# Optimization experiments

Measured on AMD Instinct MI355X. Metric: run time of the kernel, lower is better.

The kernel has to match this reference:

```python
import jax, jax.numpy as jnp
import numpy as np

N_NODES = 100000
N_EDGES = 1600000
N_GRAPHS = 512
IN_CH = 128
HID = 128
OUT_CH = 1
FP_DIM = 2048


def prelu(x, a):
    return jnp.where(x > 0, x, a * x)


def setup_inputs() -> dict:
    key = jax.random.key(0)
    ks = jax.random.split(key, 16)

    def glorot(k, shape):
        lim = np.sqrt(6.0 / (shape[0] + shape[1]))
        return jax.random.uniform(k, shape, jnp.float32, -lim, lim)

    x = jax.random.normal(ks[0], (N_NODES, IN_CH), jnp.float32)
    fp = jax.random.normal(ks[1], (N_GRAPHS, FP_DIM), jnp.float32)
    edge_index = jax.random.randint(ks[2], (2, N_EDGES), 0, N_NODES, jnp.int64)
    batch = jnp.sort(jax.random.randint(ks[3], (N_NODES,), 0, N_GRAPHS, jnp.int64))

    params = {
        "W_pre": glorot(ks[4], (IN_CH, HID)),
        "b_pre": jnp.zeros((HID,), jnp.float32),
        "a_pre": jnp.full((HID,), 0.25, jnp.float32),
        "Wl1": glorot(ks[5], (HID, HID)),
        "bl1": jnp.zeros((HID,), jnp.float32),
        "Wr1": glorot(ks[6], (HID, HID)),
        "a1": jnp.full((HID,), 0.25, jnp.float32),
        "Wl2": glorot(ks[7], (HID, HID)),
        "bl2": jnp.zeros((HID,), jnp.float32),
        "Wr2": glorot(ks[8], (HID, HID)),
        "a2": jnp.full((HID,), 0.25, jnp.float32),
        "W_fp": glorot(ks[9], (FP_DIM, HID)),
        "b_fp": jnp.zeros((HID,), jnp.float32),
        "a_fp": jnp.full((HID,), 0.25, jnp.float32),
        "W_post": glorot(ks[10], (2 * HID, OUT_CH)),
        "b_post": jnp.zeros((OUT_CH,), jnp.float32),
    }
    return dict(x=x, fp=fp, edge_index=edge_index, batch=batch, **params)


def sage_conv(x, src, dst, Wl, bl, Wr):
    # aggr='sum': sum messages x[src] into dst, then lin_l(agg)+bias + lin_r(x)
    agg = jax.ops.segment_sum(x[src], dst, num_segments=N_NODES)  # [N, H]
    return agg @ Wl + bl + x @ Wr


def reference(x, fp, edge_index, batch,
              W_pre, b_pre, a_pre,
              Wl1, bl1, Wr1, a1,
              Wl2, bl2, Wr2, a2,
              W_fp, b_fp, a_fp,
              W_post, b_post):
    src, dst = edge_index[0], edge_index[1]
    # pre_mp (dropout is identity at eval)
    h = prelu(x @ W_pre + b_pre, a_pre)
    # message passing
    h = prelu(sage_conv(h, src, dst, Wl1, bl1, Wr1), a1)
    h = prelu(sage_conv(h, src, dst, Wl2, bl2, Wr2), a2)
    # global mean pool over graphs
    sums = jax.ops.segment_sum(h, batch, num_segments=N_GRAPHS)  # [G, H]
    counts = jax.ops.segment_sum(jnp.ones((h.shape[0],), h.dtype), batch,
                                 num_segments=N_GRAPHS)
    pooled = sums / jnp.maximum(counts, 1.0)[:, None]
    # fingerprint head
    fp_emb = prelu(fp @ W_fp + b_fp, a_fp)
    # post mp
    out = jnp.concatenate([pooled, fp_emb], axis=1) @ W_post + b_post
    return out
```

## Files before the change

### kernel.cpp

```cpp
#include <hip/hip_runtime.h>

#define NN 100000
#define NE 1600000
#define NG 512
#define HID 128
#define FPD 2048
#define BSHIFT 8
#define NBUK ((NN + 255) >> 8)
#define BCAP 5120
#define EPB 4096
#define EPT 16

typedef _Float16 f16;
typedef __attribute__((ext_vector_type(8))) _Float16 f16x8;
typedef __attribute__((ext_vector_type(4))) float f32x4;


__global__ __launch_bounds__(256) void bucket_scatter(const int* __restrict__ src,
                                                      const int* __restrict__ dst,
                                                      int* __restrict__ bcnt,
                                                      uint2* __restrict__ bbuf, int E) {
  __shared__ int hist[NBUK];
  __shared__ int gbase[NBUK];
  __shared__ int lbase[NBUK + 1];
  __shared__ int sc[2][512];
  __shared__ uint2 stage[EPB];
  int t = threadIdx.x;
  int e0 = blockIdx.x * EPB;
  for (int i = t; i < NBUK; i += 256) hist[i] = 0;
  __syncthreads();

  int myb[EPT], myoff[EPT];
  uint2 myp[EPT];
#pragma unroll
  for (int u = 0; u < EPT; ++u) {
    int e = e0 + u * 256 + t;
    myb[u] = -1;
    if (e < E) {
      int d = dst[e];
      int b = d >> BSHIFT;
      myp[u] = make_uint2((uint)d, (uint)src[e]);
      myb[u] = b;
      myoff[u] = atomicAdd(&hist[b], 1);
    }
  }
  __syncthreads();

  sc[0][t] = (t < NBUK) ? hist[t] : 0;
  sc[0][t + 256] = (t + 256 < NBUK) ? hist[t + 256] : 0;
  int pp = 0;
  for (int off = 1; off < 512; off <<= 1) {
    __syncthreads();
    int a0 = sc[pp][t] + ((t >= off) ? sc[pp][t - off] : 0);
    int a1 = sc[pp][t + 256] + ((t + 256 >= off) ? sc[pp][t + 256 - off] : 0);
    sc[1 - pp][t] = a0;
    sc[1 - pp][t + 256] = a1;
    pp = 1 - pp;
  }
  __syncthreads();
  if (t < NBUK) lbase[t] = (t == 0) ? 0 : sc[pp][t - 1];
  if (t + 256 < NBUK) lbase[t + 256] = sc[pp][t + 255];
  if (t == 0) lbase[NBUK] = sc[pp][NBUK - 1];
  for (int i = t; i < NBUK; i += 256)
    if (hist[i] > 0) gbase[i] = atomicAdd(&bcnt[i], hist[i]);
  __syncthreads();

#pragma unroll
  for (int u = 0; u < EPT; ++u)
    if (myb[u] >= 0) stage[lbase[myb[u]] + myoff[u]] = myp[u];
  __syncthreads();

  int total = lbase[NBUK];
  for (int j = t; j < total; j += 256) {
    int lo = 0, hi = NBUK - 1;
    while (lo < hi) {
      int mid = (lo + hi + 1) >> 1;
      if (lbase[mid] <= j) lo = mid; else hi = mid - 1;
    }
    bbuf[(size_t)lo * BCAP + gbase[lo] + (j - lbase[lo])] = stage[j];
  }
}

__global__ __launch_bounds__(256) void bucket_hist(const int* __restrict__ bcnt,
                                                   const uint2* __restrict__ bbuf,
                                                   int* __restrict__ cnt) {
  __shared__ int h[256];
  int b = blockIdx.x, t = threadIdx.x;
  h[t] = 0;
  __syncthreads();
  int n = bcnt[b];
  const uint2* bb = bbuf + (size_t)b * BCAP;
  for (int e = t; e < n; e += 256) atomicAdd(&h[bb[e].x & 255], 1);
  __syncthreads();
  int node = (b << BSHIFT) + t;
  if (node < NN) cnt[node] = h[t];
}

__global__ __launch_bounds__(256) void scan1_kernel(const int* __restrict__ cnt,
                                                    int* __restrict__ partial,
                                                    int* __restrict__ bsums, int n) {
  __shared__ int lds[256];
  int t = threadIdx.x;
  int base = blockIdx.x * 1024 + t * 4;
  int4 v = make_int4(0, 0, 0, 0);
  if (base + 3 < n) {
    v = *reinterpret_cast<const int4*>(&cnt[base]);
  } else {
    if (base     < n) v.x = cnt[base];
    if (base + 1 < n) v.y = cnt[base + 1];
    if (base + 2 < n) v.z = cnt[base + 2];
    if (base + 3 < n) v.w = cnt[base + 3];
  }
  int s = v.x + v.y + v.z + v.w;
  lds[t] = s;
  __syncthreads();
  for (int off = 1; off < 256; off <<= 1) {
    int add = (t >= off) ? lds[t - off] : 0;
    __syncthreads();
    lds[t] += add;
    __syncthreads();
  }
  int run = lds[t] - s;
  run += v.x; if (base     < n) partial[base]     = run;
  run += v.y; if (base + 1 < n) partial[base + 1] = run;
  run += v.z; if (base + 2 < n) partial[base + 2] = run;
  run += v.w; if (base + 3 < n) partial[base + 3] = run;
  if (t == 255) bsums[blockIdx.x] = lds[255];
}

__global__ __launch_bounds__(256) void scan2_kernel(int* __restrict__ bsums, int nb) {
  __shared__ int lds[256];
  int t = threadIdx.x;
  int s = (t < nb) ? bsums[t] : 0;
  lds[t] = s;
  __syncthreads();
  for (int off = 1; off < 256; off <<= 1) {
    int add = (t >= off) ? lds[t - off] : 0;
    __syncthreads();
    lds[t] += add;
    __syncthreads();
  }
  if (t < nb) bsums[t] = lds[t] - s;
}

__global__ __launch_bounds__(256) void scan3_kernel(const int* __restrict__ partial,
                                                    const int* __restrict__ bsums,
                                                    int* __restrict__ rowptr, int n) {
  int i = blockIdx.x * 256 + threadIdx.x;
  if (i == 0) rowptr[0] = 0;
  if (i < n) rowptr[i + 1] = partial[i] + bsums[i >> 10];
}

__global__ __launch_bounds__(256) void bucket_place(const int* __restrict__ bcnt,
                                                    const uint2* __restrict__ bbuf,
                                                    const int* __restrict__ rowptr,
                                                    int* __restrict__ cols) {
  __shared__ int cur[256];
  int b = blockIdx.x, t = threadIdx.x;
  int node = (b << BSHIFT) + t;
  cur[t] = rowptr[node < NN ? node : NN];
  __syncthreads();
  int n = bcnt[b];
  const uint2* bb = bbuf + (size_t)b * BCAP;
  for (int e = t; e < n; e += 256) {
    uint2 p = bb[e];
    int pos = atomicAdd(&cur[p.x & 255], 1);
    cols[pos] = (int)p.y;
  }
}


__global__ __launch_bounds__(256) void cvt_f32_f16(const float* __restrict__ x,
                                                   f16* __restrict__ xh, int n4) {
  int i = blockIdx.x * 256 + threadIdx.x;
  if (i < n4) {
    float4 v = *reinterpret_cast<const float4*>(&x[i * 4]);
    union { uint2 u; f16 h[4]; } o;
    o.h[0] = (f16)v.x; o.h[1] = (f16)v.y; o.h[2] = (f16)v.z; o.h[3] = (f16)v.w;
    *reinterpret_cast<uint2*>(&xh[i * 4]) = o.u;
  }
}

__global__ __launch_bounds__(256) void cvt_w5(const float* __restrict__ w0,
                                              const float* __restrict__ w1,
                                              const float* __restrict__ w2,
                                              const float* __restrict__ w3,
                                              const float* __restrict__ w4,
                                              f16* __restrict__ out) {
  int idx = blockIdx.x * 256 + threadIdx.x;
  if (idx >= 5 * 16384) return;
  int w = idx >> 14, rem = idx & 16383;
  int j = rem >> 7, k = rem & 127;
  const float* W = (w == 0) ? w0 : (w == 1) ? w1 : (w == 2) ? w2 : (w == 3) ? w3 : w4;
  out[idx] = (f16)W[k * 128 + j];
}

__global__ __launch_bounds__(256) void cvt_wfp(const float* __restrict__ W,
                                               f16* __restrict__ out) {
  int idx = blockIdx.x * 256 + threadIdx.x;
  if (idx >= 128 * 2048) return;
  int j = idx >> 11, k = idx & 2047;
  out[idx] = (f16)W[k * 128 + j];
}


__global__ __launch_bounds__(256) void agg_f16(const f16* __restrict__ H,
                                               const int* __restrict__ rowptr,
                                               const int* __restrict__ cols,
                                               f16* __restrict__ out) {
  int node = blockIdx.x * 4 + (threadIdx.x >> 6);
  int lane = threadIdx.x & 63;
  int s = rowptr[node], e = rowptr[node + 1];
  float a0 = 0.f, a1 = 0.f;
  union { uint u; f16 h[2]; } cv;
  int i = s;
  for (; i + 3 < e; i += 4) {
    int c0 = cols[i], c1 = cols[i + 1], c2 = cols[i + 2], c3 = cols[i + 3];
    uint u0 = *reinterpret_cast<const uint*>(&H[(size_t)c0 * 128 + lane * 2]);
    uint u1 = *reinterpret_cast<const uint*>(&H[(size_t)c1 * 128 + lane * 2]);
    uint u2 = *reinterpret_cast<const uint*>(&H[(size_t)c2 * 128 + lane * 2]);
    uint u3 = *reinterpret_cast<const uint*>(&H[(size_t)c3 * 128 + lane * 2]);
    cv.u = u0; a0 += (float)cv.h[0]; a1 += (float)cv.h[1];
    cv.u = u1; a0 += (float)cv.h[0]; a1 += (float)cv.h[1];
    cv.u = u2; a0 += (float)cv.h[0]; a1 += (float)cv.h[1];
    cv.u = u3; a0 += (float)cv.h[0]; a1 += (float)cv.h[1];
  }
  for (; i < e; ++i) {
    cv.u = *reinterpret_cast<const uint*>(&H[(size_t)cols[i] * 128 + lane * 2]);
    a0 += (float)cv.h[0]; a1 += (float)cv.h[1];
  }
  union { uint u; f16 h[2]; } pk;
  pk.h[0] = (f16)a0; pk.h[1] = (f16)a1;
  *reinterpret_cast<uint*>(&out[(size_t)node * 128 + lane * 2]) = pk.u;
}


template <int MODE>
__global__ __launch_bounds__(256) void gemm_f16(const f16* __restrict__ A1,
                                                const f16* __restrict__ A2,
                                                const f16* __restrict__ W1t,
                                                const f16* __restrict__ W2t,
                                                const float* __restrict__ bias,
                                                const float* __restrict__ pa,
                                                f16* __restrict__ Ch, int rows) {
  int t = threadIdx.x;
  int wave = t >> 6, lane = t & 63;
  int lrow = lane & 15, lk = lane >> 4;
  int r0 = blockIdx.x * 128;
  int n0 = wave << 1;

  const f16x8* Wv1 = reinterpret_cast<const f16x8*>(W1t);
  const f16x8* Wv2 = reinterpret_cast<const f16x8*>(W2t);

  f16x8 w1[2][4], w2[2][4];
#pragma unroll
  for (int ni = 0; ni < 2; ++ni)
#pragma unroll
    for (int ks = 0; ks < 4; ++ks) {
      int wi = ((((n0 + ni) << 4) + lrow) << 4) + (ks << 2) + lk;
      w1[ni][ks] = Wv1[wi];
      if (MODE >= 1) w2[ni][ks] = Wv2[wi];
    }

  float bv[2], av[2];
#pragma unroll
  for (int ni = 0; ni < 2; ++ni) {
    int col = ((n0 + ni) << 4) + lrow;
    bv[ni] = bias ? bias[col] : 0.f;
    av[ni] = pa ? pa[col] : 1.f;
  }

  f16x8 aA[2][4], aB[2][4];
  {
    int r = r0 + lrow;
    if (r > rows - 1) r = rows - 1;
    size_t off = (size_t)r * 128 + (lk << 3);
#pragma unroll
    for (int ks = 0; ks < 4; ++ks) {
      aA[0][ks] = *reinterpret_cast<const f16x8*>(A1 + off + (ks << 5));
      if (MODE >= 1) aB[0][ks] = *reinterpret_cast<const f16x8*>(A2 + off + (ks << 5));
    }
  }

#pragma unroll
  for (int rg = 0; rg < 8; ++rg) {
    int cur = rg & 1, nxt = cur ^ 1;
    if (rg < 7) {
      int rn = r0 + ((rg + 1) << 4) + lrow;
      if (rn > rows - 1) rn = rows - 1;
      size_t offn = (size_t)rn * 128 + (lk << 3);
#pragma unroll
      for (int ks = 0; ks < 4; ++ks) {
        aA[nxt][ks] = *reinterpret_cast<const f16x8*>(A1 + offn + (ks << 5));
        if (MODE >= 1) aB[nxt][ks] = *reinterpret_cast<const f16x8*>(A2 + offn + (ks << 5));
      }
    }
    f32x4 acc1[2] = {(f32x4){0.f, 0.f, 0.f, 0.f}, (f32x4){0.f, 0.f, 0.f, 0.f}};
    f32x4 acc2[2] = {(f32x4){0.f, 0.f, 0.f, 0.f}, (f32x4){0.f, 0.f, 0.f, 0.f}};
#pragma unroll
    for (int ks = 0; ks < 4; ++ks) {
#pragma unroll
      for (int ni = 0; ni < 2; ++ni) {
        acc1[ni] = __builtin_amdgcn_mfma_f32_16x16x32_f16(aA[cur][ks], w1[ni][ks], acc1[ni], 0, 0, 0);
        if (MODE >= 1)
          acc2[ni] = __builtin_amdgcn_mfma_f32_16x16x32_f16(aB[cur][ks], w2[ni][ks], acc2[ni], 0, 0, 0);
      }
    }
#pragma unroll
    for (int ni = 0; ni < 2; ++ni) {
      int col = ((n0 + ni) << 4) + lrow;
#pragma unroll
      for (int j = 0; j < 4; ++j) {
        int rr = r0 + (rg << 4) + (lk << 2) + j;
        if (rr < rows) {
          float xv = acc1[ni][j] + bv[ni];
          if (MODE >= 1) xv += acc2[ni][j];
          if (pa) xv = xv > 0.f ? xv : av[ni] * xv;
          Ch[(size_t)rr * 128 + col] = (f16)xv;
        }
      }
    }
  }
}


__global__ __launch_bounds__(256) void fp_gemm(const f16* __restrict__ A,
                                               const f16* __restrict__ Wt,
                                               float* __restrict__ part) {
  int kc = blockIdx.x;
  int rb = blockIdx.y;
  int t = threadIdx.x;
  int wave = t >> 6, lane = t & 63;
  int lrow = lane & 15, lk = lane >> 4;
  int r0 = rb * 128;
  int n0 = wave << 1;

  const f16x8* Wv = reinterpret_cast<const f16x8*>(Wt);
  const f16x8* Av = reinterpret_cast<const f16x8*>(A);

  f16x8 w[2][4];
#pragma unroll
  for (int ni = 0; ni < 2; ++ni)
#pragma unroll
    for (int ks = 0; ks < 4; ++ks) {
      int j = ((n0 + ni) << 4) + lrow;
      w[ni][ks] = Wv[j * 256 + (kc << 4) + (ks << 2) + lk];
    }

#pragma unroll 2
  for (int rg = 0; rg < 8; ++rg) {
    int r = r0 + (rg << 4) + lrow;
    f16x8 a[4];
#pragma unroll
    for (int ks = 0; ks < 4; ++ks)
      a[ks] = Av[r * 256 + (kc << 4) + (ks << 2) + lk];
    f32x4 acc[2] = {(f32x4){0.f, 0.f, 0.f, 0.f}, (f32x4){0.f, 0.f, 0.f, 0.f}};
#pragma unroll
    for (int ks = 0; ks < 4; ++ks)
#pragma unroll
      for (int ni = 0; ni < 2; ++ni)
        acc[ni] = __builtin_amdgcn_mfma_f32_16x16x32_f16(a[ks], w[ni][ks], acc[ni], 0, 0, 0);
#pragma unroll
    for (int ni = 0; ni < 2; ++ni) {
      int col = ((n0 + ni) << 4) + lrow;
#pragma unroll
      for (int j = 0; j < 4; ++j) {
        int rr = r0 + (rg << 4) + (lk << 2) + j;
        part[((size_t)kc * 512 + rr) * 128 + col] = acc[ni][j];
      }
    }
  }
}

__global__ __launch_bounds__(256) void fp_fin(const float* __restrict__ part,
                                              const float* __restrict__ bfp,
                                              const float* __restrict__ afp,
                                              float* __restrict__ femb) {
  int idx = blockIdx.x * 256 + threadIdx.x;
  if (idx >= 512 * 128) return;
  int j = idx & 127;
  float s = bfp[j];
#pragma unroll
  for (int kc = 0; kc < 16; ++kc) s += part[(size_t)kc * 65536 + idx];
  float a = afp[j];
  femb[idx] = s > 0.f ? s : a * s;
}


__device__ __forceinline__ int lower_bound_dev(const int* __restrict__ arr, int n, int val) {
  int lo = 0, hi = n;
  while (lo < hi) {
    int mid = (lo + hi) >> 1;
    if (arr[mid] < val) lo = mid + 1; else hi = mid;
  }
  return lo;
}

__global__ __launch_bounds__(512) void pool_mean(const f16* __restrict__ H,
                                                 const int* __restrict__ batch,
                                                 float* __restrict__ pooled) {
  __shared__ float red[512];
  int g = blockIdx.x;
  int t = threadIdx.x;
  int col = t & 127, rq = t >> 7;
  int start = lower_bound_dev(batch, NN, g);
  int end = lower_bound_dev(batch, NN, g + 1);
  float acc = 0.f;
  for (int r = start + rq; r < end; r += 4) acc += (float)H[(size_t)r * 128 + col];
  red[t] = acc;
  __syncthreads();
  if (rq == 0) {
    float s = red[col] + red[128 + col] + red[256 + col] + red[384 + col];
    int c = end - start;
    pooled[g * 128 + col] = s / (float)(c > 0 ? c : 1);
  }
}


__global__ __launch_bounds__(64) void final_out(const float* __restrict__ pooled,
                                                const float* __restrict__ femb,
                                                const float* __restrict__ Wp,
                                                const float* __restrict__ bp,
                                                float* __restrict__ out) {
  int g = blockIdx.x;
  int t = threadIdx.x;
  float acc = 0.f;
  for (int i = t; i < 128; i += 64)
    acc += pooled[g * 128 + i] * Wp[i] + femb[g * 128 + i] * Wp[128 + i];
  for (int off = 32; off > 0; off >>= 1) acc += __shfl_down(acc, off);
  if (t == 0) out[g] = acc + bp[0];
}


extern "C" void kernel_launch(void* const* d_in, const int* in_sizes, int n_in,
                              void* d_out, int out_size, void* d_ws, size_t ws_size,
                              hipStream_t stream) {
  const float* x      = (const float*)d_in[0];
  const float* fp     = (const float*)d_in[1];
  const int*   ei     = (const int*)d_in[2];
  const int*   batch  = (const int*)d_in[3];
  const float* W_pre  = (const float*)d_in[4];
  const float* b_pre  = (const float*)d_in[5];
  const float* a_pre  = (const float*)d_in[6];
  const float* Wl1    = (const float*)d_in[7];
  const float* bl1    = (const float*)d_in[8];
  const float* Wr1    = (const float*)d_in[9];
  const float* a1     = (const float*)d_in[10];
  const float* Wl2    = (const float*)d_in[11];
  const float* bl2    = (const float*)d_in[12];
  const float* Wr2    = (const float*)d_in[13];
  const float* a2     = (const float*)d_in[14];
  const float* W_fp   = (const float*)d_in[15];
  const float* b_fp   = (const float*)d_in[16];
  const float* a_fp   = (const float*)d_in[17];
  const float* W_post = (const float*)d_in[18];
  const float* b_post = (const float*)d_in[19];

  const int* src = ei;
  const int* dst = ei + NE;

  const size_t NBUF = (size_t)NN * 128;
  f16* buf0 = (f16*)d_ws;
  f16* buf1 = buf0 + NBUF;
  f16* buf2 = buf1 + NBUF;
  f16* buf3 = buf2 + NBUF;
  f16* Wt   = buf3 + NBUF;
  f16* fpb  = Wt + 5 * 16384;
  f16* Wfpt = fpb + 512 * 2048;
  float* part = (float*)(Wfpt + 128 * 2048);
  int* cnt     = (int*)(part + 16 * 512 * 128);
  int* rowptr  = cnt + NN;
  int* bsums   = rowptr + NN + 4;
  int* partial = bsums + 128;
  int* colsA   = partial + NN;
  int* bcnt    = colsA + NE;
  uint2* bbuf  = (uint2*)(bcnt + ((NBUK + 3) & ~3));
  float* pooled = (float*)(bbuf + (size_t)NBUK * BCAP);
  float* femb   = pooled + NG * 128;

  hipMemsetAsync(bcnt, 0, NBUK * sizeof(int), stream);
  bucket_scatter<<<(NE + EPB - 1) / EPB, 256, 0, stream>>>(src, dst, bcnt, bbuf, NE);
  bucket_hist<<<NBUK, 256, 0, stream>>>(bcnt, bbuf, cnt);
  int nb = (NN + 1023) / 1024;
  scan1_kernel<<<nb, 256, 0, stream>>>(cnt, partial, bsums, NN);
  scan2_kernel<<<1, 256, 0, stream>>>(bsums, nb);
  scan3_kernel<<<(NN + 255) / 256, 256, 0, stream>>>(partial, bsums, rowptr, NN);
  bucket_place<<<NBUK, 256, 0, stream>>>(bcnt, bbuf, rowptr, colsA);

  cvt_f32_f16<<<(NN * 128 / 4 + 255) / 256, 256, 0, stream>>>(x, buf0, NN * 128 / 4);
  cvt_w5<<<(5 * 16384 + 255) / 256, 256, 0, stream>>>(W_pre, Wl1, Wr1, Wl2, Wr2, Wt);
  cvt_f32_f16<<<(512 * 2048 / 4 + 255) / 256, 256, 0, stream>>>(fp, fpb, 512 * 2048 / 4);
  cvt_wfp<<<(128 * 2048 + 255) / 256, 256, 0, stream>>>(W_fp, Wfpt);

  const f16* Wt_pre = Wt;
  const f16* Wt_l1  = Wt + 16384;
  const f16* Wt_r1  = Wt + 32768;
  const f16* Wt_l2  = Wt + 49152;
  const f16* Wt_r2  = Wt + 65536;

  int gGemm = (NN + 127) / 128;

  gemm_f16<0><<<gGemm, 256, 0, stream>>>(buf0, nullptr, Wt_pre, nullptr,
                                         b_pre, a_pre, buf2, NN);

  {
    dim3 g(16, 4);
    fp_gemm<<<g, 256, 0, stream>>>(fpb, Wfpt, part);
    fp_fin<<<(512 * 128 + 255) / 256, 256, 0, stream>>>(part, b_fp, a_fp, femb);
  }

  agg_f16<<<NN / 4, 256, 0, stream>>>(buf2, rowptr, colsA, buf1);
  gemm_f16<1><<<gGemm, 256, 0, stream>>>(buf1, buf2, Wt_l1, Wt_r1,
                                         bl1, a1, buf3, NN);

  agg_f16<<<NN / 4, 256, 0, stream>>>(buf3, rowptr, colsA, buf0);
  gemm_f16<1><<<gGemm, 256, 0, stream>>>(buf0, buf3, Wt_l2, Wt_r2,
                                         bl2, a2, buf2, NN);

  pool_mean<<<NG, 512, 0, stream>>>(buf2, batch, pooled);
  final_out<<<NG, 64, 0, stream>>>(pooled, femb, W_post, b_post, (float*)d_out);
}
```

Baseline: 362.9 us.

## Fuse SAGE aggregation with its GEMM and fold input conversion into pre-GEMM

Each SAGEConv layer now runs as one kernel. Every block gathers neighbor sums for 64 nodes into swizzled LDS, then runs the Wl/Wr MFMA products with bias and PReLU, so the aggregated feature matrix never goes through global memory. The pre-MLP GEMM reads fp32 x directly and converts to fp16 in registers, which removes a separate conversion pass. Bucket entries are packed into 32 bits (8-bit local dst, 24-bit src), halving bucket buffer traffic but limiting node ids to fewer than 2^24. Smaller conv blocks and the loss of prefetch in the pre-GEMM may reduce overlap.

```diff
diff --git a/kernel.cpp b/kernel.cpp
--- a/kernel.cpp
+++ b/kernel.cpp
@@ -19,19 +19,19 @@
 __global__ __launch_bounds__(256) void bucket_scatter(const int* __restrict__ src,
                                                       const int* __restrict__ dst,
                                                       int* __restrict__ bcnt,
-                                                      uint2* __restrict__ bbuf, int E) {
+                                                      uint* __restrict__ bbuf, int E) {
   __shared__ int hist[NBUK];
   __shared__ int gbase[NBUK];
   __shared__ int lbase[NBUK + 1];
   __shared__ int sc[2][512];
-  __shared__ uint2 stage[EPB];
+  __shared__ uint stage[EPB];
   int t = threadIdx.x;
   int e0 = blockIdx.x * EPB;
   for (int i = t; i < NBUK; i += 256) hist[i] = 0;
   __syncthreads();
 
   int myb[EPT], myoff[EPT];
-  uint2 myp[EPT];
+  uint myp[EPT];
 #pragma unroll
   for (int u = 0; u < EPT; ++u) {
     int e = e0 + u * 256 + t;
@@ -39,7 +39,7 @@
     if (e < E) {
       int d = dst[e];
       int b = d >> BSHIFT;
-      myp[u] = make_uint2((uint)d, (uint)src[e]);
+      myp[u] = ((uint)(d & 255) << 24) | (uint)src[e];
       myb[u] = b;
       myoff[u] = atomicAdd(&hist[b], 1);
     }
@@ -82,15 +82,15 @@
 }
 
 __global__ __launch_bounds__(256) void bucket_hist(const int* __restrict__ bcnt,
-                                                   const uint2* __restrict__ bbuf,
+                                                   const uint* __restrict__ bbuf,
                                                    int* __restrict__ cnt) {
   __shared__ int h[256];
   int b = blockIdx.x, t = threadIdx.x;
   h[t] = 0;
   __syncthreads();
   int n = bcnt[b];
-  const uint2* bb = bbuf + (size_t)b * BCAP;
-  for (int e = t; e < n; e += 256) atomicAdd(&h[bb[e].x & 255], 1);
+  const uint* bb = bbuf + (size_t)b * BCAP;
+  for (int e = t; e < n; e += 256) atomicAdd(&h[bb[e] >> 24], 1);
   __syncthreads();
   int node = (b << BSHIFT) + t;
   if (node < NN) cnt[node] = h[t];
@@ -152,7 +152,7 @@
 }
 
 __global__ __launch_bounds__(256) void bucket_place(const int* __restrict__ bcnt,
-                                                    const uint2* __restrict__ bbuf,
+                                                    const uint* __restrict__ bbuf,
                                                     const int* __restrict__ rowptr,
                                                     int* __restrict__ cols) {
   __shared__ int cur[256];
@@ -161,11 +161,11 @@
   cur[t] = rowptr[node < NN ? node : NN];
   __syncthreads();
   int n = bcnt[b];
-  const uint2* bb = bbuf + (size_t)b * BCAP;
+  const uint* bb = bbuf + (size_t)b * BCAP;
   for (int e = t; e < n; e += 256) {
-    uint2 p = bb[e];
-    int pos = atomicAdd(&cur[p.x & 255], 1);
-    cols[pos] = (int)p.y;
+    uint w = bb[e];
+    int pos = atomicAdd(&cur[w >> 24], 1);
+    cols[pos] = (int)(w & 0xFFFFFF);
   }
 }
 
@@ -204,108 +204,54 @@
 }
 
 
-__global__ __launch_bounds__(256) void agg_f16(const f16* __restrict__ H,
-                                               const int* __restrict__ rowptr,
-                                               const int* __restrict__ cols,
-                                               f16* __restrict__ out) {
-  int node = blockIdx.x * 4 + (threadIdx.x >> 6);
-  int lane = threadIdx.x & 63;
-  int s = rowptr[node], e = rowptr[node + 1];
-  float a0 = 0.f, a1 = 0.f;
-  union { uint u; f16 h[2]; } cv;
-  int i = s;
-  for (; i + 3 < e; i += 4) {
-    int c0 = cols[i], c1 = cols[i + 1], c2 = cols[i + 2], c3 = cols[i + 3];
-    uint u0 = *reinterpret_cast<const uint*>(&H[(size_t)c0 * 128 + lane * 2]);
-    uint u1 = *reinterpret_cast<const uint*>(&H[(size_t)c1 * 128 + lane * 2]);
-    uint u2 = *reinterpret_cast<const uint*>(&H[(size_t)c2 * 128 + lane * 2]);
-    uint u3 = *reinterpret_cast<const uint*>(&H[(size_t)c3 * 128 + lane * 2]);
-    cv.u = u0; a0 += (float)cv.h[0]; a1 += (float)cv.h[1];
-    cv.u = u1; a0 += (float)cv.h[0]; a1 += (float)cv.h[1];
-    cv.u = u2; a0 += (float)cv.h[0]; a1 += (float)cv.h[1];
-    cv.u = u3; a0 += (float)cv.h[0]; a1 += (float)cv.h[1];
-  }
-  for (; i < e; ++i) {
-    cv.u = *reinterpret_cast<const uint*>(&H[(size_t)cols[i] * 128 + lane * 2]);
-    a0 += (float)cv.h[0]; a1 += (float)cv.h[1];
-  }
-  union { uint u; f16 h[2]; } pk;
-  pk.h[0] = (f16)a0; pk.h[1] = (f16)a1;
-  *reinterpret_cast<uint*>(&out[(size_t)node * 128 + lane * 2]) = pk.u;
-}
-
-
-template <int MODE>
-__global__ __launch_bounds__(256) void gemm_f16(const f16* __restrict__ A1,
-                                                const f16* __restrict__ A2,
-                                                const f16* __restrict__ W1t,
-                                                const f16* __restrict__ W2t,
+__global__ __launch_bounds__(256) void gemm_pre(const float* __restrict__ X,
+                                                const f16* __restrict__ Wt,
                                                 const float* __restrict__ bias,
                                                 const float* __restrict__ pa,
-                                                f16* __restrict__ Ch, int rows) {
+                                                f16* __restrict__ out, int rows) {
   int t = threadIdx.x;
   int wave = t >> 6, lane = t & 63;
   int lrow = lane & 15, lk = lane >> 4;
   int r0 = blockIdx.x * 128;
   int n0 = wave << 1;
 
-  const f16x8* Wv1 = reinterpret_cast<const f16x8*>(W1t);
-  const f16x8* Wv2 = reinterpret_cast<const f16x8*>(W2t);
-
-  f16x8 w1[2][4], w2[2][4];
+  const f16x8* Wv = reinterpret_cast<const f16x8*>(Wt);
+  f16x8 w[2][4];
 #pragma unroll
   for (int ni = 0; ni < 2; ++ni)
 #pragma unroll
-    for (int ks = 0; ks < 4; ++ks) {
-      int wi = ((((n0 + ni) << 4) + lrow) << 4) + (ks << 2) + lk;
-      w1[ni][ks] = Wv1[wi];
-      if (MODE >= 1) w2[ni][ks] = Wv2[wi];
-    }
+    for (int ks = 0; ks < 4; ++ks)
+      w[ni][ks] = Wv[((((n0 + ni) << 4) + lrow) << 4) + (ks << 2) + lk];
 
   float bv[2], av[2];
 #pragma unroll
   for (int ni = 0; ni < 2; ++ni) {
     int col = ((n0 + ni) << 4) + lrow;
-    bv[ni] = bias ? bias[col] : 0.f;
-    av[ni] = pa ? pa[col] : 1.f;
-  }
-
-  f16x8 aA[2][4], aB[2][4];
-  {
-    int r = r0 + lrow;
+    bv[ni] = bias[col];
+    av[ni] = pa[col];
+  }
+
+#pragma unroll 2
+  for (int rg = 0; rg < 8; ++rg) {
+    int r = r0 + (rg << 4) + lrow;
     if (r > rows - 1) r = rows - 1;
-    size_t off = (size_t)r * 128 + (lk << 3);
+    const float* xp = X + (size_t)r * 128 + (lk << 3);
+    f16x8 a[4];
 #pragma unroll
     for (int ks = 0; ks < 4; ++ks) {
-      aA[0][ks] = *reinterpret_cast<const f16x8*>(A1 + off + (ks << 5));
-      if (MODE >= 1) aB[0][ks] = *reinterpret_cast<const f16x8*>(A2 + off + (ks << 5));
-    }
-  }
-
-#pragma unroll
-  for (int rg = 0; rg < 8; ++rg) {
-    int cur = rg & 1, nxt = cur ^ 1;
-    if (rg < 7) {
-      int rn = r0 + ((rg + 1) << 4) + lrow;
-      if (rn > rows - 1) rn = rows - 1;
-      size_t offn = (size_t)rn * 128 + (lk << 3);
-#pragma unroll
-      for (int ks = 0; ks < 4; ++ks) {
-        aA[nxt][ks] = *reinterpret_cast<const f16x8*>(A1 + offn + (ks << 5));
-        if (MODE >= 1) aB[nxt][ks] = *reinterpret_cast<const f16x8*>(A2 + offn + (ks << 5));
-      }
-    }
-    f32x4 acc1[2] = {(f32x4){0.f, 0.f, 0.f, 0.f}, (f32x4){0.f, 0.f, 0.f, 0.f}};
-    f32x4 acc2[2] = {(f32x4){0.f, 0.f, 0.f, 0.f}, (f32x4){0.f, 0.f, 0.f, 0.f}};
-#pragma unroll
-    for (int ks = 0; ks < 4; ++ks) {
-#pragma unroll
-      for (int ni = 0; ni < 2; ++ni) {
-        acc1[ni] = __builtin_amdgcn_mfma_f32_16x16x32_f16(aA[cur][ks], w1[ni][ks], acc1[ni], 0, 0, 0);
-        if (MODE >= 1)
-          acc2[ni] = __builtin_amdgcn_mfma_f32_16x16x32_f16(aB[cur][ks], w2[ni][ks], acc2[ni], 0, 0, 0);
-      }
-    }
+      float4 v0 = *reinterpret_cast<const float4*>(xp + (ks << 5));
+      float4 v1 = *reinterpret_cast<const float4*>(xp + (ks << 5) + 4);
+      f16x8 av8;
+      av8[0] = (f16)v0.x; av8[1] = (f16)v0.y; av8[2] = (f16)v0.z; av8[3] = (f16)v0.w;
+      av8[4] = (f16)v1.x; av8[5] = (f16)v1.y; av8[6] = (f16)v1.z; av8[7] = (f16)v1.w;
+      a[ks] = av8;
+    }
+    f32x4 acc[2] = {(f32x4){0.f, 0.f, 0.f, 0.f}, (f32x4){0.f, 0.f, 0.f, 0.f}};
+#pragma unroll
+    for (int ks = 0; ks < 4; ++ks)
+#pragma unroll
+      for (int ni = 0; ni < 2; ++ni)
+        acc[ni] = __builtin_amdgcn_mfma_f32_16x16x32_f16(a[ks], w[ni][ks], acc[ni], 0, 0, 0);
 #pragma unroll
     for (int ni = 0; ni < 2; ++ni) {
       int col = ((n0 + ni) << 4) + lrow;
@@ -313,11 +259,106 @@
       for (int j = 0; j < 4; ++j) {
         int rr = r0 + (rg << 4) + (lk << 2) + j;
         if (rr < rows) {
-          float xv = acc1[ni][j] + bv[ni];
-          if (MODE >= 1) xv += acc2[ni][j];
-          if (pa) xv = xv > 0.f ? xv : av[ni] * xv;
-          Ch[(size_t)rr * 128 + col] = (f16)xv;
+          float xv = acc[ni][j] + bv[ni];
+          xv = xv > 0.f ? xv : av[ni] * xv;
+          out[(size_t)rr * 128 + col] = (f16)xv;
         }
+      }
+    }
+  }
+}
+
+
+__global__ __launch_bounds__(512) void conv_f16(const f16* __restrict__ H,
+                                                const int* __restrict__ rowptr,
+                                                const int* __restrict__ cols,
+                                                const f16* __restrict__ Wlt,
+                                                const f16* __restrict__ Wrt,
+                                                const float* __restrict__ bias,
+                                                const float* __restrict__ pa,
+                                                f16* __restrict__ out, int rows) {
+  __shared__ __align__(16) char lds[64 * 256];
+  int t = threadIdx.x;
+  int wave = t >> 6, lane = t & 63;
+  int r0 = blockIdx.x * 64;
+
+  union { uint u; f16 h[2]; } cv;
+#pragma unroll 1
+  for (int i = 0; i < 8; ++i) {
+    int rl = (wave << 3) + i;
+    int node = r0 + rl;
+    float a0 = 0.f, a1 = 0.f;
+    if (node < rows) {
+      int s = rowptr[node], e = rowptr[node + 1];
+      int j = s;
+      for (; j + 3 < e; j += 4) {
+        int c0 = cols[j], c1 = cols[j + 1], c2 = cols[j + 2], c3 = cols[j + 3];
+        uint u0 = *reinterpret_cast<const uint*>(&H[(size_t)c0 * 128 + lane * 2]);
+        uint u1 = *reinterpret_cast<const uint*>(&H[(size_t)c1 * 128 + lane * 2]);
+        uint u2 = *reinterpret_cast<const uint*>(&H[(size_t)c2 * 128 + lane * 2]);
+        uint u3 = *reinterpret_cast<const uint*>(&H[(size_t)c3 * 128 + lane * 2]);
+        cv.u = u0; a0 += (float)cv.h[0]; a1 += (float)cv.h[1];
+        cv.u = u1; a0 += (float)cv.h[0]; a1 += (float)cv.h[1];
+        cv.u = u2; a0 += (float)cv.h[0]; a1 += (float)cv.h[1];
+        cv.u = u3; a0 += (float)cv.h[0]; a1 += (float)cv.h[1];
+      }
+      for (; j < e; ++j) {
+        cv.u = *reinterpret_cast<const uint*>(&H[(size_t)cols[j] * 128 + lane * 2]);
+        a0 += (float)cv.h[0]; a1 += (float)cv.h[1];
+      }
+    }
+    union { uint u; f16 h[2]; } pk;
+    pk.h[0] = (f16)a0; pk.h[1] = (f16)a1;
+    int byte = (rl << 8) + (lane << 2);
+    byte ^= (rl & 7) << 4;
+    *reinterpret_cast<uint*>(lds + byte) = pk.u;
+  }
+  __syncthreads();
+
+  int lrow = lane & 15, lk = lane >> 4;
+  const f16x8* Wvl = reinterpret_cast<const f16x8*>(Wlt);
+  const f16x8* Wvr = reinterpret_cast<const f16x8*>(Wrt);
+  f16x8 wl[4], wr[4];
+#pragma unroll
+  for (int ks = 0; ks < 4; ++ks) {
+    int wi = (((wave << 4) + lrow) << 4) + (ks << 2) + lk;
+    wl[ks] = Wvl[wi];
+    wr[ks] = Wvr[wi];
+  }
+  int col = (wave << 4) + lrow;
+  float bv = bias[col], av = pa[col];
+
+#pragma unroll
+  for (int rg = 0; rg < 4; ++rg) {
+    int rl = (rg << 4) + lrow;
+    f16x8 a1[4];
+#pragma unroll
+    for (int ks = 0; ks < 4; ++ks) {
+      int byte = (rl << 8) + (ks << 6) + (lk << 4);
+      byte ^= (rl & 7) << 4;
+      a1[ks] = *reinterpret_cast<const f16x8*>(lds + byte);
+    }
+    int r = r0 + rl;
+    if (r > rows - 1) r = rows - 1;
+    size_t off = (size_t)r * 128 + (lk << 3);
+    f16x8 a2[4];
+#pragma unroll
+    for (int ks = 0; ks < 4; ++ks)
+      a2[ks] = *reinterpret_cast<const f16x8*>(H + off + (ks << 5));
+    f32x4 acc1 = (f32x4){0.f, 0.f, 0.f, 0.f};
+    f32x4 acc2 = (f32x4){0.f, 0.f, 0.f, 0.f};
+#pragma unroll
+    for (int ks = 0; ks < 4; ++ks) {
+      acc1 = __builtin_amdgcn_mfma_f32_16x16x32_f16(a1[ks], wl[ks], acc1, 0, 0, 0);
+      acc2 = __builtin_amdgcn_mfma_f32_16x16x32_f16(a2[ks], wr[ks], acc2, 0, 0, 0);
+    }
+#pragma unroll
+    for (int j = 0; j < 4; ++j) {
+      int rr = r0 + (rg << 4) + (lk << 2) + j;
+      if (rr < rows) {
+        float xv = acc1[j] + acc2[j] + bv;
+        xv = xv > 0.f ? xv : av * xv;
+        out[(size_t)rr * 128 + col] = (f16)xv;
       }
     }
   }
@@ -460,11 +501,9 @@
   const int* dst = ei + NE;
 
   const size_t NBUF = (size_t)NN * 128;
-  f16* buf0 = (f16*)d_ws;
-  f16* buf1 = buf0 + NBUF;
-  f16* buf2 = buf1 + NBUF;
-  f16* buf3 = buf2 + NBUF;
-  f16* Wt   = buf3 + NBUF;
+  f16* bufA = (f16*)d_ws;
+  f16* bufB = bufA + NBUF;
+  f16* Wt   = bufB + NBUF;
   f16* fpb  = Wt + 5 * 16384;
   f16* Wfpt = fpb + 512 * 2048;
   float* part = (float*)(Wfpt + 128 * 2048);
@@ -474,7 +513,7 @@
   int* partial = bsums + 128;
   int* colsA   = partial + NN;
   int* bcnt    = colsA + NE;
-  uint2* bbuf  = (uint2*)(bcnt + ((NBUK + 3) & ~3));
+  uint* bbuf   = (uint*)(bcnt + ((NBUK + 3) & ~3));
   float* pooled = (float*)(bbuf + (size_t)NBUK * BCAP);
   float* femb   = pooled + NG * 128;
 
@@ -487,10 +526,14 @@
   scan3_kernel<<<(NN + 255) / 256, 256, 0, stream>>>(partial, bsums, rowptr, NN);
   bucket_place<<<NBUK, 256, 0, stream>>>(bcnt, bbuf, rowptr, colsA);
 
-  cvt_f32_f16<<<(NN * 128 / 4 + 255) / 256, 256, 0, stream>>>(x, buf0, NN * 128 / 4);
   cvt_w5<<<(5 * 16384 + 255) / 256, 256, 0, stream>>>(W_pre, Wl1, Wr1, Wl2, Wr2, Wt);
   cvt_f32_f16<<<(512 * 2048 / 4 + 255) / 256, 256, 0, stream>>>(fp, fpb, 512 * 2048 / 4);
   cvt_wfp<<<(128 * 2048 + 255) / 256, 256, 0, stream>>>(W_fp, Wfpt);
+  {
+    dim3 g(16, 4);
+    fp_gemm<<<g, 256, 0, stream>>>(fpb, Wfpt, part);
+    fp_fin<<<(512 * 128 + 255) / 256, 256, 0, stream>>>(part, b_fp, a_fp, femb);
+  }
 
   const f16* Wt_pre = Wt;
   const f16* Wt_l1  = Wt + 16384;
@@ -498,25 +541,14 @@
   const f16* Wt_l2  = Wt + 49152;
   const f16* Wt_r2  = Wt + 65536;
 
-  int gGemm = (NN + 127) / 128;
-
-  gemm_f16<0><<<gGemm, 256, 0, stream>>>(buf0, nullptr, Wt_pre, nullptr,
-                                         b_pre, a_pre, buf2, NN);
-
-  {
-    dim3 g(16, 4);
-    fp_gemm<<<g, 256, 0, stream>>>(fpb, Wfpt, part);
-    fp_fin<<<(512 * 128 + 255) / 256, 256, 0, stream>>>(part, b_fp, a_fp, femb);
-  }
-
-  agg_f16<<<NN / 4, 256, 0, stream>>>(buf2, rowptr, colsA, buf1);
-  gemm_f16<1><<<gGemm, 256, 0, stream>>>(buf1, buf2, Wt_l1, Wt_r1,
-                                         bl1, a1, buf3, NN);
-
-  agg_f16<<<NN / 4, 256, 0, stream>>>(buf3, rowptr, colsA, buf0);
-  gemm_f16<1><<<gGemm, 256, 0, stream>>>(buf0, buf3, Wt_l2, Wt_r2,
-                                         bl2, a2, buf2, NN);
-
-  pool_mean<<<NG, 512, 0, stream>>>(buf2, batch, pooled);
+  gemm_pre<<<(NN + 127) / 128, 256, 0, stream>>>(x, Wt_pre, b_pre, a_pre, bufA, NN);
+
+  int gConv = (NN + 63) / 64;
+
+  conv_f16<<<gConv, 512, 0, stream>>>(bufA, rowptr, colsA, Wt_l1, Wt_r1, bl1, a1, bufB, NN);
+
+  conv_f16<<<gConv, 512, 0, stream>>>(bufB, rowptr, colsA, Wt_l2, Wt_r2, bl2, a2, bufA, NN);
+
+  pool_mean<<<NG, 512, 0, stream>>>(bufA, batch, pooled);
   final_out<<<NG, 64, 0, stream>>>(pooled, femb, W_post, b_post, (float*)d_out);
 }
```

Result: slower. 416.1 us (+14.6%).
